# Optimization experiments

Hardware: AMD Instinct MI355X
Metric: run time of the kernel (lower is better)

## Reference

```python
import jax, jax.numpy as jnp
import numpy as np

B, T, V, D, H, A = 256, 512, 50000, 256, 256, 128


def setup_inputs() -> dict:
    key = jax.random.key(0)
    ks = jax.random.split(key, 9)
    x = jax.random.randint(ks[0], (B, T), 0, V, dtype=jnp.int32)
    embed_w = jax.random.uniform(ks[1], (V, D), dtype=jnp.float32)          # random_uniform init, non-trainable
    lstm_kernel = jax.random.normal(ks[2], (D + H, 4 * H), dtype=jnp.float32) * 0.05  # BasicLSTMCell kernel [i,j,f,o]
    lstm_bias = jnp.zeros((4 * H,), jnp.float32)
    w_omega = jax.random.normal(ks[3], (H, A), dtype=jnp.float32)
    b_omega = jax.random.normal(ks[4], (A,), dtype=jnp.float32)
    u_omega = jax.random.normal(ks[5], (A,), dtype=jnp.float32)
    w = jax.random.normal(ks[6], (H, 2), dtype=jnp.float32)
    b = jnp.zeros((2,), jnp.float32)
    return {"x": x, "embed_w": embed_w, "lstm_kernel": lstm_kernel,
            "lstm_bias": lstm_bias, "w_omega": w_omega, "b_omega": b_omega,
            "u_omega": u_omega, "w": w, "b": b}


def _lstm_attention_forward(x, embed_w, lstm_kernel, lstm_bias, w_omega, b_omega, u_omega, w, b):
    Bt, Tt = x.shape
    Hh = lstm_bias.shape[0] // 4
    seq_len = jnp.sum(jnp.sign(x), axis=1)                         # [B] like tf.reduce_sum(tf.sign(x))
    e = embed_w[x]                                                  # [B,T,D] embedding lookup
    # dynamic_rnn semantics: outputs zeroed past seq_len, state frozen
    mask = (jnp.arange(Tt)[:, None] < seq_len[None, :]).astype(e.dtype)  # [T,B]
    xs = (jnp.transpose(e, (1, 0, 2)), mask[:, :, None])            # time-major

    def step(carry, inp):
        c, h = carry
        x_t, m = inp                                                # [B,D], [B,1]
        z = jnp.concatenate([x_t, h], axis=-1) @ lstm_kernel + lstm_bias  # [B,4H]
        i, j, f, o = jnp.split(z, 4, axis=-1)
        c_new = c * jax.nn.sigmoid(f + 1.0) + jax.nn.sigmoid(i) * jnp.tanh(j)  # forget_bias=1.0
        h_new = jnp.tanh(c_new) * jax.nn.sigmoid(o)
        c = jnp.where(m > 0, c_new, c)
        h_out = h_new * m
        h = jnp.where(m > 0, h_new, h)
        return (c, h), h_out

    c0 = jnp.zeros((Bt, Hh), e.dtype)
    h0 = jnp.zeros((Bt, Hh), e.dtype)
    _, outs = jax.lax.scan(step, (c0, h0), xs)                      # [T,B,H]
    outs = jnp.transpose(outs, (1, 0, 2))                           # [B,T,H]

    # additive attention pooling
    value = jnp.tanh(jnp.einsum('bth,ha->bta', outs, w_omega) + b_omega)
    vu = jnp.einsum('bta,a->bt', value, u_omega)
    alphas = jax.nn.softmax(vu, axis=-1)                            # [B,T]
    last = jnp.sum(outs * alphas[..., None], axis=1)                # [B,H]

    logits = last @ w + b                                           # [B,2]
    return jax.nn.softmax(logits)


def reference(x, embed_w, lstm_kernel, lstm_bias, w_omega, b_omega, u_omega, w, b):
    return _lstm_attention_forward(x, embed_w, lstm_kernel, lstm_bias,
                                   w_omega, b_omega, u_omega, w, b)
```

## Files before the change

kernel.cpp:

```cpp
#include <hip/hip_runtime.h>
#include <hip/hip_bf16.h>
#include <cstdint>
#include <cstddef>

typedef _Float16 f16;
typedef _Float16 f16x8 __attribute__((ext_vector_type(8)));
typedef _Float16 f16x4 __attribute__((ext_vector_type(4)));
typedef float f32x4 __attribute__((ext_vector_type(4)));
typedef unsigned long long u64;
typedef unsigned int u32;

#define B_   256
#define T_   512
#define V_   50000
#define D_   256
#define H_   256
#define A_   128
#define N4H  1024

__device__ __forceinline__ float sigmoid_f(float x) {
    return __builtin_amdgcn_rcpf(1.f + __expf(-x));
}
__device__ __forceinline__ float tanh_f(float x) {
    float e = __expf(-2.f * fabsf(x));
    float t = 1.f - 2.f * e * __builtin_amdgcn_rcpf(1.f + e);
    return copysignf(t, x);
}

#define MFMA_A(accv, afragv, bfraga)                                         \
    asm volatile("v_mfma_f32_16x16x32_f16 %0, %1, %2, %0"                    \
                 : "+v"(accv) : "v"(afragv), "a"(bfraga))

#define LGKM_BARRIER()                                                       \
    do {                                                                     \
        asm volatile("s_waitcnt lgkmcnt(0)" ::: "memory");                   \
        __builtin_amdgcn_sched_barrier(0);                                   \
        __builtin_amdgcn_s_barrier();                                        \
        __builtin_amdgcn_sched_barrier(0);                                   \
    } while (0)

__global__ __launch_bounds__(256) void k0_convert(
    const float* __restrict__ lstm_kernel, const float* __restrict__ w_omega,
    f16* __restrict__ WxT, f16* __restrict__ WhT, f16* __restrict__ WomT) {
    int blk = blockIdx.x;
    int tau = threadIdx.x;
    if (blk < N4H) {
        int n = blk;
        WxT[n * 256 + tau] = (f16)lstm_kernel[(size_t)tau * N4H + n];
        WhT[n * 256 + tau] = (f16)lstm_kernel[(size_t)(256 + tau) * N4H + n];
    } else {
        int a = blk - N4H;
        WomT[a * 256 + tau] = (f16)w_omega[(size_t)tau * A_ + a];
    }
}

__global__ __launch_bounds__(256) void k1_seqlen(
    const int* __restrict__ x, int* __restrict__ seqlen) {
    __shared__ int red[256];
    int b = blockIdx.x, tau = threadIdx.x;
    int cnt = (x[b * T_ + tau] != 0) + (x[b * T_ + tau + 256] != 0);
    red[tau] = cnt;
    __syncthreads();
    for (int s = 128; s > 0; s >>= 1) {
        if (tau < s) red[tau] += red[tau + s];
        __syncthreads();
    }
    if (tau == 0) seqlen[b] = red[0];
}

__global__ __launch_bounds__(256) void k2_zx(
    const int* __restrict__ x, const float* __restrict__ embed,
    const f16* __restrict__ WxT, const float* __restrict__ bias,
    f16* __restrict__ Zx, int t0, int Tc) {
    __shared__ __align__(16) f16 A_s[64][264];
    __shared__ __align__(16) f16 B_s[128][72];
    __shared__ int tok_s[64];

    int tau  = threadIdx.x;
    int bm   = blockIdx.x;
    int i0   = bm * 64;
    int wave = tau >> 6, lane = tau & 63;
    int q = lane >> 4, c = lane & 15;

    if (tau < 64) {
        int i  = i0 + tau;
        int bb = i / Tc, tr = i - bb * Tc;
        tok_s[tau] = x[bb * T_ + t0 + tr];
    }
    __syncthreads();

    {
        int r = tau >> 2, quarter = tau & 3;
        const float4* src =
            (const float4*)(embed + (size_t)tok_s[r] * D_ + quarter * 64);
        f16* dst = &A_s[r][quarter * 64];
#pragma unroll
        for (int j = 0; j < 16; j++) {
            float4 v = src[j];
            dst[j * 4 + 0] = (f16)v.x;
            dst[j * 4 + 1] = (f16)v.y;
            dst[j * 4 + 2] = (f16)v.z;
            dst[j * 4 + 3] = (f16)v.w;
        }
    }

    for (int np = 0; np < 8; np++) {
        f32x4 acc[8];
#pragma unroll
        for (int ni = 0; ni < 8; ni++) acc[ni] = (f32x4){0.f, 0.f, 0.f, 0.f};

        for (int kt = 0; kt < 4; kt++) {
            __syncthreads();
            {
                int n = tau >> 1, half = tau & 1;
                const f16x8* src = (const f16x8*)(WxT +
                    (size_t)(np * 128 + n) * 256 + kt * 64 + half * 32);
                f16x8* dst = (f16x8*)&B_s[n][half * 32];
#pragma unroll
                for (int j = 0; j < 4; j++) dst[j] = src[j];
            }
            __syncthreads();
#pragma unroll
            for (int s = 0; s < 2; s++) {
                f16x8 afrag =
                    *(const f16x8*)&A_s[wave * 16 + c][kt * 64 + s * 32 + q * 8];
#pragma unroll
                for (int ni = 0; ni < 8; ni++) {
                    f16x8 bfrag = *(const f16x8*)&B_s[ni * 16 + c][s * 32 + q * 8];
                    acc[ni] = __builtin_amdgcn_mfma_f32_16x16x32_f16(
                        afrag, bfrag, acc[ni], 0, 0, 0);
                }
            }
        }
#pragma unroll
        for (int ni = 0; ni < 8; ni++) {
            int n    = np * 128 + ni * 16 + c;
            int g    = n >> 8, rem = n & 255;
            int half = rem >> 7, colu = rem & 127;
            int np2  = half * 512 + colu * 4 + g;
            float bv = bias[n];
#pragma unroll
            for (int r = 0; r < 4; r++) {
                int row = i0 + wave * 16 + q * 4 + r;
                Zx[(size_t)row * N4H + np2] = (f16)(acc[ni][r] + bv);
            }
        }
    }
}

__global__ __launch_bounds__(512, 2) void k3_lstm(
    const f16* __restrict__ Zx, const f16* __restrict__ WhT,
    const int* __restrict__ seqlen, f16* __restrict__ outs,
    f16* __restrict__ Hstate, float* __restrict__ Cstate,
    u32* __restrict__ Hex, int t0, int Tc, int first, int last) {
    __shared__ __align__(16) f16 Zx_s[2][16][520];
    __shared__ __align__(16) f16 h_s[2][16][264];

    int tau  = threadIdx.x;
    int w    = tau >> 6, lane = tau & 63;
    int q = lane >> 4, c = lane & 15;
    int wgid = blockIdx.x;
    int pair = wgid >> 1, half = wgid & 1;
    int b0 = pair * 16;
    int u0 = half * 128, pu0 = (half ^ 1) * 128;
    int u  = u0 + w * 16 + c;
    int col = w * 16 + c;

    u32* hexw_my = Hex + (size_t)wgid * 2 * 2048;
    u32* hexw_pr = Hex + (size_t)(wgid ^ 1) * 2 * 2048;

    f32x4 wha[4][8];
#pragma unroll
    for (int g = 0; g < 4; g++)
#pragma unroll
        for (int s = 0; s < 8; s++) {
            int kc = (s < 4) ? (half * 4 + s) : ((half ^ 1) * 4 + (s - 4));
            f16x8 f = *(const f16x8*)(WhT +
                (size_t)(g * 256 + u0 + w * 16 + c) * 256 + kc * 32 + q * 8);
            f32x4 t = __builtin_bit_cast(f32x4, f);
            asm volatile("" : "=a"(wha[g][s]) : "0"(t));
        }

    int kOwn = half * 128 + q * 8;
    int kPar = (half ^ 1) * 128 + q * 8;

    int p0 = t0 & 1;
    if (first) {
        for (int idx = tau; idx < 2 * 16 * 264; idx += 512)
            ((f16*)h_s)[idx] = (f16)0.f;
    } else {
        for (int idx = tau; idx < 16 * 256; idx += 512) {
            int r = idx >> 8, k = idx & 255;
            h_s[p0][r][k] = Hstate[(b0 + r) * H_ + k];
        }
    }

    float cst[4];
    f16   hprev[4];
    int   sl[4];
#pragma unroll
    for (int r = 0; r < 4; r++) {
        int row = q * 4 + r;
        cst[r]   = first ? 0.f : Cstate[(b0 + row) * H_ + u];
        hprev[r] = first ? (f16)0.f : Hstate[(b0 + row) * H_ + u];
        sl[r]    = seqlen[b0 + row];
    }

    int r_st = tau >> 5;
    int cc   = (tau & 31) * 16;
    const f16* zxrow = Zx + ((size_t)(b0 + r_st) * Tc) * N4H + half * 512 + cc;

    {
        const f16x8* src = (const f16x8*)zxrow;
        f16x8* dst = (f16x8*)&Zx_s[p0][r_st][cc];
        dst[0] = src[0];
        dst[1] = src[1];
    }
    int rr = tau >> 5;
    int uu = (tau & 31) * 4;

    __syncthreads();

    f32x4 accO[4];
#pragma unroll
    for (int g = 0; g < 4; g++) accO[g] = (f32x4){0.f, 0.f, 0.f, 0.f};
#pragma unroll
    for (int kk = 0; kk < 4; kk++) {
        f16x8 afrag = *(const f16x8*)&h_s[p0][c][kOwn + kk * 32];
#pragma unroll
        for (int g = 0; g < 4; g++) MFMA_A(accO[g], afrag, wha[g][kk]);
    }

    u64 vp0 = 0, vp1 = 0;

    for (int tt = 0; tt < Tc; tt++) {
        int t   = t0 + tt;
        int cur = t & 1, nxt = cur ^ 1;

        int tn = (tt + 1 < Tc) ? tt + 1 : tt;
        const f16x8* psrc = (const f16x8*)(zxrow + (size_t)tn * N4H);
        f16x8 z0 = psrc[0];
        f16x8 z1 = psrc[1];

        if (tt > 0) {
            u32 tagp = (u32)(t & 0xffff);
            const u64* pp = (const u64*)&hexw_pr[cur * 2048 + rr * 128 + uu];
            while (((u32)(vp0 >> 16) & 0xffffu) != tagp ||
                   ((u32)(vp0 >> 48)) != tagp ||
                   ((u32)(vp1 >> 16) & 0xffffu) != tagp ||
                   ((u32)(vp1 >> 48)) != tagp) {
                vp0 = __hip_atomic_load(pp + 0, __ATOMIC_RELAXED,
                                        __HIP_MEMORY_SCOPE_AGENT);
                vp1 = __hip_atomic_load(pp + 1, __ATOMIC_RELAXED,
                                        __HIP_MEMORY_SCOPE_AGENT);
            }
            u64 hw = (u64)(vp0 & 0xffff) | (((vp0 >> 32) & 0xffff) << 16) |
                     ((vp1 & 0xffff) << 32) | (((vp1 >> 32) & 0xffff) << 48);
            *(u64*)&h_s[cur][rr][pu0 + uu] = hw;
        }
        LGKM_BARRIER();

#pragma unroll
        for (int kk = 0; kk < 4; kk++) {
            f16x8 afrag = *(const f16x8*)&h_s[cur][c][kPar + kk * 32];
#pragma unroll
            for (int g = 0; g < 4; g++) MFMA_A(accO[g], afrag, wha[g][4 + kk]);
        }

        u32 tag = (u32)((t + 1) & 0xffff);
        f16 ovals[4];
#pragma unroll
        for (int r = 0; r < 4; r++) {
            int row = q * 4 + r;
            f16x4 zv = *(const f16x4*)&Zx_s[cur][row][col * 4];
            float zi = accO[0][r] + (float)zv[0];
            float zj = accO[1][r] + (float)zv[1];
            float zf = accO[2][r] + (float)zv[2];
            float zo = accO[3][r] + (float)zv[3];
            float ig = sigmoid_f(zi);
            float jg = tanh_f(zj);
            float fg = sigmoid_f(zf + 1.f);
            float og = sigmoid_f(zo);
            float cn = cst[r] * fg + ig * jg;
            float hn = tanh_f(cn) * og;
            bool  m  = (t < sl[r]);
            cst[r]   = m ? cn : cst[r];
            f16 hkeep = m ? (f16)hn : hprev[r];
            hprev[r]  = hkeep;
            h_s[nxt][row][u] = hkeep;
            u32 word = (tag << 16) |
                       (u32)(unsigned short)__builtin_bit_cast(short, hkeep);
            __hip_atomic_store(&hexw_my[nxt * 2048 + row * 128 + col], word,
                               __ATOMIC_RELAXED, __HIP_MEMORY_SCOPE_AGENT);
            ovals[r] = m ? (f16)hn : (f16)0.f;
        }

        {
            const u64* pp2 = (const u64*)&hexw_pr[nxt * 2048 + rr * 128 + uu];
            vp0 = __hip_atomic_load(pp2 + 0, __ATOMIC_RELAXED,
                                    __HIP_MEMORY_SCOPE_AGENT);
            vp1 = __hip_atomic_load(pp2 + 1, __ATOMIC_RELAXED,
                                    __HIP_MEMORY_SCOPE_AGENT);
        }

        {
            f16x8* dst = (f16x8*)&Zx_s[nxt][r_st][cc];
            dst[0] = z0;
            dst[1] = z1;
        }

#pragma unroll
        for (int r = 0; r < 4; r++)
            outs[((size_t)(b0 + q * 4 + r) * T_ + t) * H_ + u] = ovals[r];

        LGKM_BARRIER();

#pragma unroll
        for (int g = 0; g < 4; g++) accO[g] = (f32x4){0.f, 0.f, 0.f, 0.f};
#pragma unroll
        for (int kk = 0; kk < 4; kk++) {
            f16x8 afrag = *(const f16x8*)&h_s[nxt][c][kOwn + kk * 32];
#pragma unroll
            for (int g = 0; g < 4; g++) MFMA_A(accO[g], afrag, wha[g][kk]);
        }
    }

    if (!last) {
        int parity = (t0 + Tc) & 1;
        for (int idx = tau; idx < 16 * 128; idx += 512) {
            int r = idx >> 7, k = u0 + (idx & 127);
            Hstate[(b0 + r) * H_ + k] = h_s[parity][r][k];
        }
#pragma unroll
        for (int r = 0; r < 4; r++)
            Cstate[(b0 + q * 4 + r) * H_ + u] = cst[r];
    }
}

__global__ __launch_bounds__(256) void k4_attn(
    const f16* __restrict__ outs, const f16* __restrict__ WomT,
    const float* __restrict__ b_omega, const float* __restrict__ u_omega,
    const float* __restrict__ w, const float* __restrict__ bfin,
    float* __restrict__ out) {
    __shared__ __align__(16) f16 A_s[64][264];
    __shared__ __align__(16) f16 val_s[64][132];
    __shared__ float u_s[128];
    __shared__ float vu_s[512];
    __shared__ float red0[256], red1[256];

    int b = blockIdx.x, tau = threadIdx.x;
    int wave = tau >> 6, lane = tau & 63;
    int q = lane >> 4, c = lane & 15;

    if (tau < 128) u_s[tau] = u_omega[tau];
    float bom[8];
#pragma unroll
    for (int ni = 0; ni < 8; ni++) bom[ni] = b_omega[ni * 16 + c];

    for (int ch = 0; ch < 8; ch++) {
        int t0c = ch * 64;
        __syncthreads();
        {
            int r = tau >> 2, seg = tau & 3;
            const f16x8* src =
                (const f16x8*)(outs + ((size_t)b * T_ + t0c + r) * H_ + seg * 64);
            f16x8* dst = (f16x8*)&A_s[r][seg * 64];
#pragma unroll
            for (int j = 0; j < 8; j++) dst[j] = src[j];
        }
        __syncthreads();

        f32x4 acc[8];
#pragma unroll
        for (int ni = 0; ni < 8; ni++) acc[ni] = (f32x4){0.f, 0.f, 0.f, 0.f};
#pragma unroll
        for (int kc = 0; kc < 8; kc++) {
            f16x8 afrag = *(const f16x8*)&A_s[wave * 16 + c][kc * 32 + q * 8];
#pragma unroll
            for (int ni = 0; ni < 8; ni++) {
                f16x8 bfrag = *(const f16x8*)(WomT +
                    (size_t)(ni * 16 + c) * 256 + kc * 32 + q * 8);
                acc[ni] = __builtin_amdgcn_mfma_f32_16x16x32_f16(
                    afrag, bfrag, acc[ni], 0, 0, 0);
            }
        }
#pragma unroll
        for (int ni = 0; ni < 8; ni++) {
#pragma unroll
            for (int r = 0; r < 4; r++) {
                val_s[wave * 16 + q * 4 + r][ni * 16 + c] =
                    (f16)tanh_f(acc[ni][r] + bom[ni]);
            }
        }
        __syncthreads();
        if (tau < 64) {
            float s = 0.f;
#pragma unroll 8
            for (int a = 0; a < 128; a++) s += (float)val_s[tau][a] * u_s[a];
            vu_s[t0c + tau] = s;
        }
    }
    __syncthreads();

    red0[tau] = fmaxf(vu_s[tau], vu_s[tau + 256]);
    __syncthreads();
    for (int s = 128; s > 0; s >>= 1) {
        if (tau < s) red0[tau] = fmaxf(red0[tau], red0[tau + s]);
        __syncthreads();
    }
    float mx = red0[0];
    __syncthreads();
    float e0 = __expf(vu_s[tau] - mx), e1 = __expf(vu_s[tau + 256] - mx);
    red0[tau] = e0 + e1;
    __syncthreads();
    for (int s = 128; s > 0; s >>= 1) {
        if (tau < s) red0[tau] += red0[tau + s];
        __syncthreads();
    }
    float inv = 1.f / red0[0];
    __syncthreads();
    vu_s[tau]       = e0 * inv;
    vu_s[tau + 256] = e1 * inv;
    __syncthreads();

    float lastv = 0.f;
#pragma unroll 4
    for (int t = 0; t < T_; t++)
        lastv += vu_s[t] * (float)outs[((size_t)b * T_ + t) * H_ + tau];

    red0[tau] = lastv * w[tau * 2 + 0];
    red1[tau] = lastv * w[tau * 2 + 1];
    __syncthreads();
    for (int s = 128; s > 0; s >>= 1) {
        if (tau < s) {
            red0[tau] += red0[tau + s];
            red1[tau] += red1[tau + s];
        }
        __syncthreads();
    }
    if (tau == 0) {
        float l0 = red0[0] + bfin[0], l1 = red1[0] + bfin[1];
        float mm = fmaxf(l0, l1);
        float a0 = __expf(l0 - mm), a1 = __expf(l1 - mm);
        float den = a0 + a1;
        out[b * 2 + 0] = a0 / den;
        out[b * 2 + 1] = a1 / den;
    }
}

extern "C" void kernel_launch(void* const* d_in, const int* in_sizes, int n_in,
                              void* d_out, int out_size, void* d_ws,
                              size_t ws_size, hipStream_t stream) {
    const int*   x           = (const int*)d_in[0];
    const float* embed       = (const float*)d_in[1];
    const float* lstm_kernel = (const float*)d_in[2];
    const float* lstm_bias   = (const float*)d_in[3];
    const float* w_omega     = (const float*)d_in[4];
    const float* b_omega     = (const float*)d_in[5];
    const float* u_omega     = (const float*)d_in[6];
    const float* w           = (const float*)d_in[7];
    const float* bfin        = (const float*)d_in[8];
    float*       out         = (float*)d_out;

    char* ws = (char*)d_ws;
    f16*   WxT    = (f16*)(ws + 0);
    f16*   WhT    = (f16*)(ws + 524288);
    f16*   WomT   = (f16*)(ws + 1048576);
    int*   seqlen = (int*)(ws + 1114112);
    f16*   Hstate = (f16*)(ws + 1115136);
    float* Cstate = (float*)(ws + 1246208);
    u32*   Hex    = (u32*)(ws + 1508352);
    f16*   outs   = (f16*)(ws + 2032640);
    f16*   Zx     = (f16*)(ws + 2032640 + 67108864);

    const size_t fixed = 2032640ull + 67108864ull;
    int nch = 1;
    while (nch < 16 && fixed + 268435456ull / (size_t)nch > ws_size) nch <<= 1;
    int Tc = T_ / nch;

    k0_convert<<<1152, 256, 0, stream>>>(lstm_kernel, w_omega, WxT, WhT, WomT);
    k1_seqlen<<<256, 256, 0, stream>>>(x, seqlen);
    for (int chk = 0; chk < nch; chk++) {
        int t0 = chk * Tc;
        k2_zx<<<(B_ * Tc) / 64, 256, 0, stream>>>(x, embed, WxT, lstm_bias, Zx,
                                                  t0, Tc);
        k3_lstm<<<32, 512, 0, stream>>>(Zx, WhT, seqlen, outs, Hstate, Cstate,
                                        Hex, t0, Tc, chk == 0 ? 1 : 0,
                                        chk == nch - 1 ? 1 : 0);
    }
    k4_attn<<<256, 256, 0, stream>>>(outs, WomT, b_omega, u_omega, w, bfin, out);
}
```

Before: 1.585 ms.

## Overlap next-chunk Zx input projection with LSTM recurrence via extra producer blocks

Adds producer workgroups to the LSTM recurrence kernel that compute the embedding-times-Wx projection for the next time chunk into a double-buffered Zx buffer. The recurrence itself uses only 32 workgroups, so the rest of the GPU can work on the next chunk's projection in parallel instead of waiting for a separate serialized k2 launch. It also moves the Zx shared-memory store and the outs global store ahead of the partner h-exchange loads, to hide that latency. The cost is twice the Zx workspace, which may force more chunks, and producer blocks competing with the latency-critical recurrence blocks for memory bandwidth and CU resources.

New measurement: 1.447 ms. 8.7% less time.

```diff
diff --git a/kernel.cpp b/kernel.cpp
--- a/kernel.cpp
+++ b/kernel.cpp
@@ -148,11 +148,98 @@
     }
 }
 
+__device__ __forceinline__ void zx_producer(
+    const int* __restrict__ x, const float* __restrict__ embed,
+    const f16* __restrict__ WxT, const float* __restrict__ bias,
+    f16* __restrict__ Zx, int pb, int t0, int Tc) {
+    __shared__ __align__(16) f16 Ap_s[128][264];
+    __shared__ __align__(16) f16 Bp_s[128][72];
+    __shared__ int tokp_s[128];
+
+    int tau  = threadIdx.x;
+    int i0   = pb * 128;
+    int wave = tau >> 6, lane = tau & 63;
+    int q = lane >> 4, c = lane & 15;
+
+    if (tau < 128) {
+        int i  = i0 + tau;
+        int bb = i / Tc, tr = i - bb * Tc;
+        tokp_s[tau] = x[bb * T_ + t0 + tr];
+    }
+    __syncthreads();
+
+    {
+        int r = tau >> 2, quarter = tau & 3;
+        const float4* src =
+            (const float4*)(embed + (size_t)tokp_s[r] * D_ + quarter * 64);
+        f16* dst = &Ap_s[r][quarter * 64];
+#pragma unroll
+        for (int j = 0; j < 16; j++) {
+            float4 v = src[j];
+            dst[j * 4 + 0] = (f16)v.x;
+            dst[j * 4 + 1] = (f16)v.y;
+            dst[j * 4 + 2] = (f16)v.z;
+            dst[j * 4 + 3] = (f16)v.w;
+        }
+    }
+
+    for (int np = 0; np < 8; np++) {
+        f32x4 acc[8];
+#pragma unroll
+        for (int ni = 0; ni < 8; ni++) acc[ni] = (f32x4){0.f, 0.f, 0.f, 0.f};
+
+        for (int kt = 0; kt < 4; kt++) {
+            __syncthreads();
+            {
+                int n = tau >> 2, qt = tau & 3;
+                const f16x8* src = (const f16x8*)(WxT +
+                    (size_t)(np * 128 + n) * 256 + kt * 64 + qt * 16);
+                f16x8* dst = (f16x8*)&Bp_s[n][qt * 16];
+                dst[0] = src[0];
+                dst[1] = src[1];
+            }
+            __syncthreads();
+#pragma unroll
+            for (int s = 0; s < 2; s++) {
+                f16x8 afrag =
+                    *(const f16x8*)&Ap_s[wave * 16 + c][kt * 64 + s * 32 + q * 8];
+#pragma unroll
+                for (int ni = 0; ni < 8; ni++) {
+                    f16x8 bfrag = *(const f16x8*)&Bp_s[ni * 16 + c][s * 32 + q * 8];
+                    acc[ni] = __builtin_amdgcn_mfma_f32_16x16x32_f16(
+                        afrag, bfrag, acc[ni], 0, 0, 0);
+                }
+            }
+        }
+#pragma unroll
+        for (int ni = 0; ni < 8; ni++) {
+            int n     = np * 128 + ni * 16 + c;
+            int g     = n >> 8, rem = n & 255;
+            int halfn = rem >> 7, colu = rem & 127;
+            int np2   = halfn * 512 + colu * 4 + g;
+            float bv  = bias[n];
+#pragma unroll
+            for (int r = 0; r < 4; r++) {
+                int row = i0 + wave * 16 + q * 4 + r;
+                Zx[(size_t)row * N4H + np2] = (f16)(acc[ni][r] + bv);
+            }
+        }
+    }
+}
+
 __global__ __launch_bounds__(512, 2) void k3_lstm(
     const f16* __restrict__ Zx, const f16* __restrict__ WhT,
     const int* __restrict__ seqlen, f16* __restrict__ outs,
     f16* __restrict__ Hstate, float* __restrict__ Cstate,
-    u32* __restrict__ Hex, int t0, int Tc, int first, int last) {
+    u32* __restrict__ Hex, int t0, int Tc, int first, int last,
+    const int* __restrict__ x, const float* __restrict__ embed,
+    const f16* __restrict__ WxT, const float* __restrict__ bias,
+    f16* __restrict__ ZxNext, int t0n) {
+    if (blockIdx.x >= 32) {
+        zx_producer(x, embed, WxT, bias, ZxNext, blockIdx.x - 32, t0n, Tc);
+        return;
+    }
+
     __shared__ __align__(16) f16 Zx_s[2][16][520];
     __shared__ __align__(16) f16 h_s[2][16][264];
 
@@ -296,22 +383,22 @@
         }
 
         {
+            f16x8* dst = (f16x8*)&Zx_s[nxt][r_st][cc];
+            dst[0] = z0;
+            dst[1] = z1;
+        }
+
+#pragma unroll
+        for (int r = 0; r < 4; r++)
+            outs[((size_t)(b0 + q * 4 + r) * T_ + t) * H_ + u] = ovals[r];
+
+        {
             const u64* pp2 = (const u64*)&hexw_pr[nxt * 2048 + rr * 128 + uu];
             vp0 = __hip_atomic_load(pp2 + 0, __ATOMIC_RELAXED,
                                     __HIP_MEMORY_SCOPE_AGENT);
             vp1 = __hip_atomic_load(pp2 + 1, __ATOMIC_RELAXED,
                                     __HIP_MEMORY_SCOPE_AGENT);
         }
-
-        {
-            f16x8* dst = (f16x8*)&Zx_s[nxt][r_st][cc];
-            dst[0] = z0;
-            dst[1] = z1;
-        }
-
-#pragma unroll
-        for (int r = 0; r < 4; r++)
-            outs[((size_t)(b0 + q * 4 + r) * T_ + t) * H_ + u] = ovals[r];
 
         LGKM_BARRIER();
 
@@ -471,22 +558,30 @@
     float* Cstate = (float*)(ws + 1246208);
     u32*   Hex    = (u32*)(ws + 1508352);
     f16*   outs   = (f16*)(ws + 2032640);
-    f16*   Zx     = (f16*)(ws + 2032640 + 67108864);
 
     const size_t fixed = 2032640ull + 67108864ull;
     int nch = 1;
-    while (nch < 16 && fixed + 268435456ull / (size_t)nch > ws_size) nch <<= 1;
+    while (nch < 16 && fixed + 2ull * (268435456ull / (size_t)nch) > ws_size)
+        nch <<= 1;
     int Tc = T_ / nch;
+    size_t chunkB = 268435456ull / (size_t)nch;
+    f16* ZxA = (f16*)(ws + fixed);
+    f16* ZxB = (f16*)(ws + fixed + chunkB);
 
     k0_convert<<<1152, 256, 0, stream>>>(lstm_kernel, w_omega, WxT, WhT, WomT);
     k1_seqlen<<<256, 256, 0, stream>>>(x, seqlen);
+    k2_zx<<<(B_ * Tc) / 64, 256, 0, stream>>>(x, embed, WxT, lstm_bias, ZxA,
+                                              0, Tc);
     for (int chk = 0; chk < nch; chk++) {
-        int t0 = chk * Tc;
-        k2_zx<<<(B_ * Tc) / 64, 256, 0, stream>>>(x, embed, WxT, lstm_bias, Zx,
-                                                  t0, Tc);
-        k3_lstm<<<32, 512, 0, stream>>>(Zx, WhT, seqlen, outs, Hstate, Cstate,
-                                        Hex, t0, Tc, chk == 0 ? 1 : 0,
-                                        chk == nch - 1 ? 1 : 0);
+        int  t0  = chk * Tc;
+        f16* zc  = (chk & 1) ? ZxB : ZxA;
+        f16* zn  = (chk & 1) ? ZxA : ZxB;
+        int  np  = (chk + 1 < nch) ? (B_ * Tc) / 128 : 0;
+        int  t0n = (chk + 1) * Tc;
+        k3_lstm<<<32 + np, 512, 0, stream>>>(
+            zc, WhT, seqlen, outs, Hstate, Cstate, Hex, t0, Tc,
+            chk == 0 ? 1 : 0, chk == nch - 1 ? 1 : 0,
+            x, embed, WxT, lstm_bias, zn, t0n);
     }
     k4_attn<<<256, 256, 0, stream>>>(outs, WomT, b_omega, u_omega, w, bfin, out);
 }
```
